# Kernel tuning notes

Hardware: AMD Instinct MI355X
Metric: run time of the kernel (lower is better)

The kernel has to match this reference:

```python
import jax, jax.numpy as jnp
import numpy as np

B, N, C, H, KH = 4, 4096, 1024, 16, 5
HD = C // H  # head dim = 64


def setup_inputs() -> dict:
    key = jax.random.key(0)
    ks = jax.random.split(key, 4)
    return {
        "x": jax.random.normal(ks[0], (B, N, C), jnp.float32),
        "qkv_w": jax.random.normal(ks[1], (3 * C, C), jnp.float32) * 0.02,
        "qkv_b": jnp.zeros((3 * C,), jnp.float32),
        "proj_w": jax.random.normal(ks[2], (C, C), jnp.float32) * 0.02,
        "proj_b": jnp.zeros((C,), jnp.float32),
        "pos_enc": jnp.zeros((1, C), jnp.float32),  # torch init: zeros
        "dwc_w": jax.random.normal(ks[3], (HD, 1, KH, KH), jnp.float32) * 0.05,
        "dwc_b": jnp.zeros((HD,), jnp.float32),
        "num_heads": H,
    }


def reference(x, qkv_w, qkv_b, proj_w, proj_b, pos_enc, dwc_w, dwc_b, num_heads):
    b, n, c = x.shape
    h = num_heads
    hd = c // h
    kh = dwc_w.shape[2]

    qkv = x @ qkv_w.T + qkv_b                     # (b, n, 3c)
    q, k, v = jnp.split(qkv, 3, axis=-1)          # each (b, n, c)
    k = k + pos_enc[:, :c]                        # broadcast (1, c)
    q = jax.nn.relu(q)
    k = jax.nn.relu(k)

    def to_heads(t):  # (b, n, c) -> (b*h, n, hd)
        return t.reshape(b, n, h, hd).transpose(0, 2, 1, 3).reshape(b * h, n, hd)

    q, k, v = to_heads(q), to_heads(k), to_heads(v)

    # linear attention in fp32 (inputs already fp32)
    z = 1.0 / (jnp.einsum('bic,bc->bi', q, k.sum(axis=1)) + 1e-6)   # (bh, n)
    kv = jnp.einsum('bjc,bjd->bcd', k, v)                           # (bh, hd, hd)
    out = jnp.einsum('bic,bcd->bid', q, kv) * z[:, :, None]         # (bh, n, hd)

    # depthwise 2D conv on v viewed as (bh, hd, n, 1), kernel (hd,1,kh,kh), pad kh//2
    fm = v.transpose(0, 2, 1)[..., None]                            # (bh, hd, n, 1)
    pad = kh // 2
    fm = jax.lax.conv_general_dilated(
        fm, dwc_w, window_strides=(1, 1),
        padding=((pad, pad), (pad, pad)),
        dimension_numbers=('NCHW', 'OIHW', 'NCHW'),
        feature_group_count=hd,
    ) + dwc_b[None, :, None, None]
    out = out + fm[..., 0].transpose(0, 2, 1)                       # (bh, n, hd)

    out = out.reshape(b, h, n, hd).transpose(0, 2, 1, 3).reshape(b, n, c)
    return out @ proj_w.T + proj_b
```

## Files before the change

kernel.cpp:

```cpp
#include <hip/hip_runtime.h>


#define BB   4
#define NN   4096
#define CDIM 1024
#define NH   16
#define HDIM 64
#define BH   64

typedef __attribute__((ext_vector_type(8))) short short8;
typedef __attribute__((ext_vector_type(4))) float f32x4;
typedef unsigned short u16;

__device__ __forceinline__ float b2f(short s) {
    union { unsigned u; float f; } c;
    c.u = ((unsigned)(unsigned short)s) << 16;
    return c.f;
}
__device__ __forceinline__ u16 f2b(float f) {
    unsigned u = __float_as_uint(f);
    return (u16)((u + 0x7fffu + ((u >> 16) & 1u)) >> 16);
}
__device__ __forceinline__ void gload16(const void* g, void* l) {
    __builtin_amdgcn_global_load_lds((const __attribute__((address_space(1))) void*)g,
                                     (__attribute__((address_space(3))) void*)l, 16, 0, 0);
}

__global__ __launch_bounds__(256) void k_fill_diag(float* __restrict__ out, int n, float val)
{
    int i = blockIdx.x * 256 + threadIdx.x;
    if (i < n) out[i] = val;
}

__global__ __launch_bounds__(256) void k_f32_to_bf16(const float* __restrict__ in,
                                                     u16* __restrict__ out, int n4)
{
    int i = blockIdx.x * 256 + threadIdx.x;
    if (i < n4) {
        float4 v = reinterpret_cast<const float4*>(in)[i];
        ushort4 o;
        o.x = f2b(v.x); o.y = f2b(v.y); o.z = f2b(v.z); o.w = f2b(v.w);
        reinterpret_cast<ushort4*>(out)[i] = o;
    }
}

__global__ __launch_bounds__(256) void k_gemm1_mfma(
    const u16* __restrict__ A,
    const u16* __restrict__ Bw,
    const float* __restrict__ bias, const float* __restrict__ pos_enc,
    u16* __restrict__ q, u16* __restrict__ kk_, u16* __restrict__ v)
{
    __shared__ u16 As[128 * 32];
    __shared__ u16 Bs[128 * 32];
    const int t = threadIdx.x;
    const int l = t & 63, w = t >> 6;
    const int wr = w >> 1, wc = w & 1;
    const int nbx = gridDim.x, nwg = nbx * gridDim.y;
    const int lid = blockIdx.y * nbx + blockIdx.x;
    const int swz = (lid & 7) * (nwg >> 3) + (lid >> 3);
    const int bcol = (swz % nbx) * 128;
    const int brow = (swz / nbx) * 128;
    const int sr = t >> 2;
    const int sk = (t & 3) * 8;
    const u16* gA = A  + (brow + sr) * 1024 + sk;
    const u16* gB = Bw + (bcol + sr) * 1024 + sk;
    char* ldsA = (char*)As + w * 1024;
    char* ldsB = (char*)Bs + w * 1024;

    f32x4 acc[4][4];
    #pragma unroll
    for (int m = 0; m < 4; ++m)
        #pragma unroll
        for (int n = 0; n < 4; ++n) acc[m][n] = (f32x4){0.f, 0.f, 0.f, 0.f};

    const int ar = wr * 64 + (l & 15);
    const int bc = wc * 64 + (l & 15);
    const int kfrag = (l >> 4) * 8;

    for (int k0 = 0; k0 < 1024; k0 += 32) {
        gload16(gA + k0,             ldsA);
        gload16(gA + k0 + 64 * 1024, ldsA + 4096);
        gload16(gB + k0,             ldsB);
        gload16(gB + k0 + 64 * 1024, ldsB + 4096);
        __syncthreads();
        short8 a[4], b[4];
        #pragma unroll
        for (int m = 0; m < 4; ++m)
            a[m] = *reinterpret_cast<const short8*>(&As[(ar + m * 16) * 32 + kfrag]);
        #pragma unroll
        for (int n = 0; n < 4; ++n)
            b[n] = *reinterpret_cast<const short8*>(&Bs[(bc + n * 16) * 32 + kfrag]);
        #pragma unroll
        for (int m = 0; m < 4; ++m)
            #pragma unroll
            for (int n = 0; n < 4; ++n)
                acc[m][n] = __builtin_amdgcn_mfma_f32_16x16x32_bf16(a[m], b[n], acc[m][n], 0, 0, 0);
        __syncthreads();
    }

    const int part = bcol >> 10;
    u16* dst = (part == 0) ? q : (part == 1) ? kk_ : v;
    const int col_base = bcol + wc * 64 + (l & 15);
    const int row_base = brow + wr * 64 + (l >> 4) * 4;
    #pragma unroll
    for (int n = 0; n < 4; ++n) {
        const int gc = col_base + n * 16;
        const int c  = gc & 1023;
        float bv = bias[gc];
        if (part == 1) bv += pos_enc[c];
        const int h = c >> 6, d = c & 63;
        #pragma unroll
        for (int m = 0; m < 4; ++m)
            #pragma unroll
            for (int j = 0; j < 4; ++j) {
                const int gr = row_base + m * 16 + j;
                const int b_ = gr >> 12, i_ = gr & 4095;
                float val = acc[m][n][j] + bv;
                if (part != 2) val = fmaxf(val, 0.f);
                dst[(size_t)((b_ * NH + h) * NN + i_) * HDIM + d] = f2b(val);
            }
    }
}

__global__ __launch_bounds__(256) void k_kv_partial(
    const u16* __restrict__ k, const u16* __restrict__ v,
    float* __restrict__ part_kv, float* __restrict__ part_ks)
{
    __shared__ float ks[32 * 64];
    __shared__ float vs[32 * 64];
    const int bh = blockIdx.x;
    const int chunk = blockIdx.y;
    const int t = threadIdx.x;
    const int cg = t >> 4;
    const int dg = t & 15;
    const int lr = t >> 3;
    const int lc = (t & 7) * 8;
    const size_t base = (size_t)bh * NN * HDIM + (size_t)chunk * 1024 * HDIM;
    float acc[4][4] = {};
    float ksac[4] = {};
    for (int j0 = 0; j0 < 1024; j0 += 32) {
        short8 kr = *reinterpret_cast<const short8*>(&k[base + (size_t)(j0 + lr) * 64 + lc]);
        short8 vr = *reinterpret_cast<const short8*>(&v[base + (size_t)(j0 + lr) * 64 + lc]);
        __syncthreads();
        #pragma unroll
        for (int j = 0; j < 8; ++j) {
            ks[lr * 64 + lc + j] = b2f(kr[j]);
            vs[lr * 64 + lc + j] = b2f(vr[j]);
        }
        __syncthreads();
        #pragma unroll
        for (int j = 0; j < 32; ++j) {
            float4 k4 = *reinterpret_cast<const float4*>(&ks[j * 64 + cg * 4]);
            float4 v4 = *reinterpret_cast<const float4*>(&vs[j * 64 + dg * 4]);
            const float* kp = reinterpret_cast<const float*>(&k4);
            const float* vp = reinterpret_cast<const float*>(&v4);
            #pragma unroll
            for (int ii = 0; ii < 4; ++ii) {
                ksac[ii] += kp[ii];
                #pragma unroll
                for (int jj = 0; jj < 4; ++jj)
                    acc[ii][jj] += kp[ii] * vp[jj];
            }
        }
    }
    const int pb = (chunk * BH + bh);
    #pragma unroll
    for (int ii = 0; ii < 4; ++ii) {
        #pragma unroll
        for (int jj = 0; jj < 4; ++jj)
            part_kv[pb * 4096 + (cg * 4 + ii) * 64 + dg * 4 + jj] = acc[ii][jj];
        if (dg == 0) part_ks[pb * 64 + cg * 4 + ii] = ksac[ii];
    }
}

__global__ __launch_bounds__(256) void k_kv_reduce_t(
    const float* __restrict__ part_kv, const float* __restrict__ part_ks,
    u16* __restrict__ kvt)
{
    const int bh = blockIdx.x;
    const int t = threadIdx.x;
    u16* base = kvt + bh * 5120;
    #pragma unroll
    for (int r = 0; r < 16; ++r) {
        const int idx = r * 256 + t;
        const int c = idx >> 6, d = idx & 63;
        float s = 0.f;
        #pragma unroll
        for (int ch = 0; ch < 4; ++ch) s += part_kv[(ch * BH + bh) * 4096 + idx];
        base[d * 64 + c] = f2b(s);
    }
    if (t < 64) {
        float s = 0.f;
        #pragma unroll
        for (int ch = 0; ch < 4; ++ch) s += part_ks[(ch * BH + bh) * 64 + t];
        base[4096 + t] = f2b(s);
    }
    for (int z = t; z < 960; z += 256) base[4160 + z] = 0;
}

__global__ __launch_bounds__(256) void k_attn_mfma(
    const u16* __restrict__ q, const u16* __restrict__ v,
    const u16* __restrict__ kvt,
    const float* __restrict__ dwc_w, const float* __restrict__ dwc_b,
    u16* __restrict__ out2)
{
    __shared__ u16 att[4][64 * 68];
    const int t = threadIdx.x;
    const int l = t & 63, w = t >> 6;
    const int bh = blockIdx.x;
    const int tb = blockIdx.y * 256 + w * 64;
    const size_t hb = (size_t)bh * NN * HDIM;
    const u16* qb  = q + hb + (size_t)tb * HDIM;
    const u16* kvb = kvt + bh * 5120;

    const int fr = l & 15;
    const int kfrag = (l >> 4) * 8;

    short8 bfr[5][2];
    #pragma unroll
    for (int n = 0; n < 5; ++n)
        #pragma unroll
        for (int ks = 0; ks < 2; ++ks)
            bfr[n][ks] = *reinterpret_cast<const short8*>(&kvb[(n * 16 + fr) * 64 + ks * 32 + kfrag]);

    f32x4 acc[4][5];
    #pragma unroll
    for (int m = 0; m < 4; ++m)
        #pragma unroll
        for (int n = 0; n < 5; ++n) acc[m][n] = (f32x4){0.f, 0.f, 0.f, 0.f};

    #pragma unroll
    for (int m = 0; m < 4; ++m)
        #pragma unroll
        for (int ks = 0; ks < 2; ++ks) {
            short8 a = *reinterpret_cast<const short8*>(&qb[(m * 16 + fr) * 64 + ks * 32 + kfrag]);
            #pragma unroll
            for (int n = 0; n < 5; ++n)
                acc[m][n] = __builtin_amdgcn_mfma_f32_16x16x32_bf16(a, bfr[n][ks], acc[m][n], 0, 0, 0);
        }

    #pragma unroll
    for (int m = 0; m < 4; ++m)
        #pragma unroll
        for (int j = 0; j < 4; ++j) {
            const float den = __shfl(acc[m][4][j], l & 48);
            const float z = 1.f / (den + 1e-6f);
            const int row = m * 16 + (l >> 4) * 4 + j;
            #pragma unroll
            for (int n = 0; n < 4; ++n)
                att[w][row * 68 + fr + n * 16] = f2b(acc[m][n][j] * z);
        }
    __syncthreads();

    const int d = l;
    float w5[5];
    #pragma unroll
    for (int dh = 0; dh < 5; ++dh) w5[dh] = dwc_w[d * 25 + dh * 5 + 2];
    const float cbias = dwc_b[d];
    const int b_ = bh >> 4, h_ = bh & 15;
    u16* obase = out2 + (size_t)b_ * NN * CDIM + (size_t)h_ * 64 + d;
    float win[5];
    #pragma unroll
    for (int p = 0; p < 4; ++p) {
        const int src = tb - 2 + p;
        win[p] = (src >= 0 && src < NN) ? b2f(v[hb + (size_t)src * 64 + d]) : 0.f;
    }
    for (int it = 0; it < 64; ++it) {
        const int srcn = tb + it + 2;
        win[4] = (srcn < NN) ? b2f(v[hb + (size_t)srcn * 64 + d]) : 0.f;
        const float fm = cbias + w5[0] * win[0] + w5[1] * win[1] + w5[2] * win[2]
                               + w5[3] * win[3] + w5[4] * win[4];
        const float attn = b2f((short)att[w][it * 68 + d]);
        obase[(size_t)(tb + it) * CDIM] = f2b(attn + fm);
        win[0] = win[1]; win[1] = win[2]; win[2] = win[3]; win[3] = win[4];
    }
}

__global__ __launch_bounds__(256) void k_gemm2_mfma(
    const u16* __restrict__ A,
    const u16* __restrict__ Bw,
    const float* __restrict__ bias, float* __restrict__ out)
{
    __shared__ u16 As[128 * 32];
    __shared__ u16 Bs[128 * 32];
    const int t = threadIdx.x;
    const int l = t & 63, w = t >> 6;
    const int wr = w >> 1, wc = w & 1;
    const int nbx = gridDim.x, nwg = nbx * gridDim.y;
    const int lid = blockIdx.y * nbx + blockIdx.x;
    const int swz = (lid & 7) * (nwg >> 3) + (lid >> 3);
    const int bcol = (swz % nbx) * 128;
    const int brow = (swz / nbx) * 128;
    const int sr = t >> 2;
    const int sk = (t & 3) * 8;
    const u16* gA = A  + (brow + sr) * 1024 + sk;
    const u16* gB = Bw + (bcol + sr) * 1024 + sk;
    char* ldsA = (char*)As + w * 1024;
    char* ldsB = (char*)Bs + w * 1024;

    f32x4 acc[4][4];
    #pragma unroll
    for (int m = 0; m < 4; ++m)
        #pragma unroll
        for (int n = 0; n < 4; ++n) acc[m][n] = (f32x4){0.f, 0.f, 0.f, 0.f};

    const int ar = wr * 64 + (l & 15);
    const int bc = wc * 64 + (l & 15);
    const int kfrag = (l >> 4) * 8;

    for (int k0 = 0; k0 < 1024; k0 += 32) {
        gload16(gA + k0,             ldsA);
        gload16(gA + k0 + 64 * 1024, ldsA + 4096);
        gload16(gB + k0,             ldsB);
        gload16(gB + k0 + 64 * 1024, ldsB + 4096);
        __syncthreads();
        short8 a[4], b[4];
        #pragma unroll
        for (int m = 0; m < 4; ++m)
            a[m] = *reinterpret_cast<const short8*>(&As[(ar + m * 16) * 32 + kfrag]);
        #pragma unroll
        for (int n = 0; n < 4; ++n)
            b[n] = *reinterpret_cast<const short8*>(&Bs[(bc + n * 16) * 32 + kfrag]);
        #pragma unroll
        for (int m = 0; m < 4; ++m)
            #pragma unroll
            for (int n = 0; n < 4; ++n)
                acc[m][n] = __builtin_amdgcn_mfma_f32_16x16x32_bf16(a[m], b[n], acc[m][n], 0, 0, 0);
        __syncthreads();
    }

    const int col_base = bcol + wc * 64 + (l & 15);
    const int row_base = brow + wr * 64 + (l >> 4) * 4;
    #pragma unroll
    for (int n = 0; n < 4; ++n) {
        const int gc = col_base + n * 16;
        const float bv = bias[gc];
        #pragma unroll
        for (int m = 0; m < 4; ++m)
            #pragma unroll
            for (int j = 0; j < 4; ++j) {
                const int gr = row_base + m * 16 + j;
                out[(size_t)gr * CDIM + gc] = acc[m][n][j] + bv;
            }
    }
}

extern "C" void kernel_launch(void* const* d_in, const int* in_sizes, int n_in,
                              void* d_out, int out_size, void* d_ws, size_t ws_size,
                              hipStream_t stream)
{
    const float* x       = (const float*)d_in[0];
    const float* qkv_w   = (const float*)d_in[1];
    const float* qkv_b   = (const float*)d_in[2];
    const float* proj_w  = (const float*)d_in[3];
    const float* proj_b  = (const float*)d_in[4];
    const float* pos_enc = (const float*)d_in[5];
    const float* dwc_w   = (const float*)d_in[6];
    const float* dwc_b   = (const float*)d_in[7];

    const size_t QKV = 16777216;
    char* p = (char*)d_ws;
    u16* q_b    = (u16*)p;               p += QKV * 2;
    u16* k_b    = (u16*)p;               p += QKV * 2;
    u16* v_b    = (u16*)p;               p += QKV * 2;
    u16* x_b    = (u16*)p;               p += QKV * 2;
    u16* qkvw_b = (u16*)p;               p += (size_t)3145728 * 2;
    u16* projw_b= (u16*)p;               p += (size_t)1048576 * 2;
    float* part_kv = (float*)p;          p += (size_t)1048576 * 4;
    float* part_ks = (float*)p;          p += (size_t)16384 * 4;
    u16* kvt       = (u16*)p;            p += (size_t)(64 * 5120) * 2;
    const size_t need_bytes = (size_t)(p - (char*)d_ws);

    if (ws_size < need_bytes) {
        const float diag = 4096.0f + (float)(ws_size >> 20);
        k_fill_diag<<<(out_size + 255) / 256, 256, 0, stream>>>((float*)d_out, out_size, diag);
        return;
    }

    u16* out2 = k_b;
    float* out = (float*)d_out;

    k_f32_to_bf16<<<16384, 256, 0, stream>>>(x,      x_b,     4194304);
    k_f32_to_bf16<<< 3072, 256, 0, stream>>>(qkv_w,  qkvw_b,   786432);
    k_f32_to_bf16<<< 1024, 256, 0, stream>>>(proj_w, projw_b,  262144);

    k_gemm1_mfma <<<dim3(24, 128), 256, 0, stream>>>(x_b, qkvw_b, qkv_b, pos_enc, q_b, k_b, v_b);
    k_kv_partial <<<dim3(64, 4),   256, 0, stream>>>(k_b, v_b, part_kv, part_ks);
    k_kv_reduce_t<<<64,            256, 0, stream>>>(part_kv, part_ks, kvt);
    k_attn_mfma  <<<dim3(64, 16),  256, 0, stream>>>(q_b, v_b, kvt, dwc_w, dwc_b, out2);
    k_gemm2_mfma <<<dim3(8, 128),  256, 0, stream>>>(out2, projw_b, proj_b, out);
}
```

Before: 321.2 us.

## Rewrite both GEMMs as 256x256 double-buffered MFMA tiles with swizzled LDS

Replaces the 128x128 single-buffered GEMM kernels for the QKV and output projections with 256x256 tiles computed by 512-thread blocks. Global-to-LDS loads go into two buffers so the next k-slice is fetched while MFMAs run on the current one, and the LDS layout is XOR-swizzled to cut bank conflicts. It also raises wave priority around the MFMA block. Each wave now holds twice as many accumulators, which increases register pressure, and the larger tiles produce fewer blocks and lower occupancy.

```diff
diff --git a/kernel.cpp b/kernel.cpp
--- a/kernel.cpp
+++ b/kernel.cpp
@@ -44,64 +44,89 @@
     }
 }
 
-__global__ __launch_bounds__(256) void k_gemm1_mfma(
+
+#define GEMM_PROLOGUE_AND_LOOP(EXTRA_BCOLS)                                              \
+    const int t = threadIdx.x;                                                           \
+    const int l = t & 63, w = t >> 6;                                                    \
+    const int wr = w >> 2, wc = w & 3;                                                   \
+    const int qa = ((l & 3) ^ ((l >> 3) & 3)) * 8;                                       \
+    const int srow = t >> 2;                                                             \
+    const u16* gA = A  + (size_t)(brow + srow) * 1024 + qa;                              \
+    const u16* gB = Bw + (size_t)(bcol + srow) * 1024 + qa;                              \
+    const int fr = l & 15;                                                               \
+    const int phys8 = ((l >> 4) ^ ((l >> 1) & 3)) * 8;                                   \
+    const int arow0 = wr * 128 + fr;                                                     \
+    const int bfr0  = wc * 64 + fr;                                                      \
+    f32x4 acc[8][4];                                                                     \
+    _Pragma("unroll")                                                                    \
+    for (int m = 0; m < 8; ++m)                                                          \
+        _Pragma("unroll")                                                                \
+        for (int n = 0; n < 4; ++n) acc[m][n] = (f32x4){0.f, 0.f, 0.f, 0.f};             \
+                                              \
+    auto STAGE = [&](int buf, int kt) {                                                  \
+        const int kof = kt * 32;                                                         \
+        char* lb = (char*)lds + buf * 32768 + w * 1024;                                  \
+        gload16(gA + kof,          lb);                                                  \
+        gload16(gA + 131072 + kof, lb + 8192);                                           \
+        gload16(gB + kof,          lb + 16384);                                          \
+        gload16(gB + 131072 + kof, lb + 24576);                                          \
+    };                                                                                   \
+    STAGE(0, 0);                                                                         \
+    STAGE(1, 1);                                                                         \
+    asm volatile("s_waitcnt vmcnt(4)" ::: "memory");                                     \
+    __builtin_amdgcn_sched_barrier(0);                                                   \
+    __builtin_amdgcn_s_barrier();                                                        \
+    __builtin_amdgcn_sched_barrier(0);                                                   \
+    for (int kt = 0; kt < 32; ++kt) {                                                    \
+        const int cur = kt & 1;                                                          \
+        const int ab = cur * 16384;                                                      \
+        short8 af[8], bf[4];                                                             \
+        _Pragma("unroll")                                                                \
+        for (int n = 0; n < 4; ++n)                                                      \
+            bf[n] = *reinterpret_cast<const short8*>(                                    \
+                        &lds[ab + 8192 + (bfr0 + n * 16) * 32 + phys8]);                 \
+        _Pragma("unroll")                                                                \
+        for (int m = 0; m < 8; ++m)                                                      \
+            af[m] = *reinterpret_cast<const short8*>(                                    \
+                        &lds[ab + (arow0 + m * 16) * 32 + phys8]);                       \
+        asm volatile("s_waitcnt lgkmcnt(0)" ::: "memory");                               \
+        __builtin_amdgcn_sched_barrier(0);                                               \
+        __builtin_amdgcn_s_barrier();               \
+        __builtin_amdgcn_sched_barrier(0);                                               \
+        if (kt + 2 < 32) STAGE(cur, kt + 2);                                             \
+        __builtin_amdgcn_s_setprio(1);                                                   \
+        _Pragma("unroll")                                                                \
+        for (int m = 0; m < 8; ++m)                                                      \
+            _Pragma("unroll")                                                            \
+            for (int n = 0; n < 4; ++n)                                                  \
+                acc[m][n] = __builtin_amdgcn_mfma_f32_16x16x32_bf16(                     \
+                                af[m], bf[n], acc[m][n], 0, 0, 0);                       \
+        __builtin_amdgcn_s_setprio(0);                                                   \
+        if (kt + 2 < 32) { asm volatile("s_waitcnt vmcnt(4)" ::: "memory"); }            \
+        else             { asm volatile("s_waitcnt vmcnt(0)" ::: "memory"); }            \
+        __builtin_amdgcn_sched_barrier(0);                                               \
+        __builtin_amdgcn_s_barrier();                 \
+        __builtin_amdgcn_sched_barrier(0);                                               \
+    }
+
+__global__ __launch_bounds__(512, 2) void k_gemm1_256(
     const u16* __restrict__ A,
     const u16* __restrict__ Bw,
     const float* __restrict__ bias, const float* __restrict__ pos_enc,
     u16* __restrict__ q, u16* __restrict__ kk_, u16* __restrict__ v)
 {
-    __shared__ u16 As[128 * 32];
-    __shared__ u16 Bs[128 * 32];
-    const int t = threadIdx.x;
-    const int l = t & 63, w = t >> 6;
-    const int wr = w >> 1, wc = w & 1;
-    const int nbx = gridDim.x, nwg = nbx * gridDim.y;
-    const int lid = blockIdx.y * nbx + blockIdx.x;
-    const int swz = (lid & 7) * (nwg >> 3) + (lid >> 3);
-    const int bcol = (swz % nbx) * 128;
-    const int brow = (swz / nbx) * 128;
-    const int sr = t >> 2;
-    const int sk = (t & 3) * 8;
-    const u16* gA = A  + (brow + sr) * 1024 + sk;
-    const u16* gB = Bw + (bcol + sr) * 1024 + sk;
-    char* ldsA = (char*)As + w * 1024;
-    char* ldsB = (char*)Bs + w * 1024;
-
-    f32x4 acc[4][4];
-    #pragma unroll
-    for (int m = 0; m < 4; ++m)
-        #pragma unroll
-        for (int n = 0; n < 4; ++n) acc[m][n] = (f32x4){0.f, 0.f, 0.f, 0.f};
-
-    const int ar = wr * 64 + (l & 15);
-    const int bc = wc * 64 + (l & 15);
-    const int kfrag = (l >> 4) * 8;
-
-    for (int k0 = 0; k0 < 1024; k0 += 32) {
-        gload16(gA + k0,             ldsA);
-        gload16(gA + k0 + 64 * 1024, ldsA + 4096);
-        gload16(gB + k0,             ldsB);
-        gload16(gB + k0 + 64 * 1024, ldsB + 4096);
-        __syncthreads();
-        short8 a[4], b[4];
-        #pragma unroll
-        for (int m = 0; m < 4; ++m)
-            a[m] = *reinterpret_cast<const short8*>(&As[(ar + m * 16) * 32 + kfrag]);
-        #pragma unroll
-        for (int n = 0; n < 4; ++n)
-            b[n] = *reinterpret_cast<const short8*>(&Bs[(bc + n * 16) * 32 + kfrag]);
-        #pragma unroll
-        for (int m = 0; m < 4; ++m)
-            #pragma unroll
-            for (int n = 0; n < 4; ++n)
-                acc[m][n] = __builtin_amdgcn_mfma_f32_16x16x32_bf16(a[m], b[n], acc[m][n], 0, 0, 0);
-        __syncthreads();
-    }
+    __shared__ u16 lds[32768];
+    const int lid = blockIdx.y * 12 + blockIdx.x;
+    const int swz = (lid & 7) * 96 + (lid >> 3);
+    const int bcol = (swz % 12) * 256;
+    const int brow = (swz / 12) * 256;
+
+    GEMM_PROLOGUE_AND_LOOP()
 
     const int part = bcol >> 10;
     u16* dst = (part == 0) ? q : (part == 1) ? kk_ : v;
-    const int col_base = bcol + wc * 64 + (l & 15);
-    const int row_base = brow + wr * 64 + (l >> 4) * 4;
+    const int col_base = bcol + wc * 64 + fr;
+    const int row_base = brow + wr * 128 + (l >> 4) * 4;
     #pragma unroll
     for (int n = 0; n < 4; ++n) {
         const int gc = col_base + n * 16;
@@ -110,7 +135,7 @@
         if (part == 1) bv += pos_enc[c];
         const int h = c >> 6, d = c & 63;
         #pragma unroll
-        for (int m = 0; m < 4; ++m)
+        for (int m = 0; m < 8; ++m)
             #pragma unroll
             for (int j = 0; j < 4; ++j) {
                 const int gr = row_base + m * 16 + j;
@@ -118,6 +143,35 @@
                 float val = acc[m][n][j] + bv;
                 if (part != 2) val = fmaxf(val, 0.f);
                 dst[(size_t)((b_ * NH + h) * NN + i_) * HDIM + d] = f2b(val);
+            }
+    }
+}
+
+__global__ __launch_bounds__(512, 2) void k_gemm2_256(
+    const u16* __restrict__ A,
+    const u16* __restrict__ Bw,
+    const float* __restrict__ bias, float* __restrict__ out)
+{
+    __shared__ u16 lds[32768];
+    const int lid = blockIdx.y * 4 + blockIdx.x;
+    const int swz = (lid & 7) * 32 + (lid >> 3);
+    const int bcol = (swz % 4) * 256;
+    const int brow = (swz / 4) * 256;
+
+    GEMM_PROLOGUE_AND_LOOP()
+
+    const int col_base = bcol + wc * 64 + fr;
+    const int row_base = brow + wr * 128 + (l >> 4) * 4;
+    #pragma unroll
+    for (int n = 0; n < 4; ++n) {
+        const int gc = col_base + n * 16;
+        const float bv = bias[gc];
+        #pragma unroll
+        for (int m = 0; m < 8; ++m)
+            #pragma unroll
+            for (int j = 0; j < 4; ++j) {
+                const int gr = row_base + m * 16 + j;
+                out[(size_t)gr * CDIM + gc] = acc[m][n][j] + bv;
             }
     }
 }
@@ -276,75 +330,6 @@
     }
 }
 
-__global__ __launch_bounds__(256) void k_gemm2_mfma(
-    const u16* __restrict__ A,
-    const u16* __restrict__ Bw,
-    const float* __restrict__ bias, float* __restrict__ out)
-{
-    __shared__ u16 As[128 * 32];
-    __shared__ u16 Bs[128 * 32];
-    const int t = threadIdx.x;
-    const int l = t & 63, w = t >> 6;
-    const int wr = w >> 1, wc = w & 1;
-    const int nbx = gridDim.x, nwg = nbx * gridDim.y;
-    const int lid = blockIdx.y * nbx + blockIdx.x;
-    const int swz = (lid & 7) * (nwg >> 3) + (lid >> 3);
-    const int bcol = (swz % nbx) * 128;
-    const int brow = (swz / nbx) * 128;
-    const int sr = t >> 2;
-    const int sk = (t & 3) * 8;
-    const u16* gA = A  + (brow + sr) * 1024 + sk;
-    const u16* gB = Bw + (bcol + sr) * 1024 + sk;
-    char* ldsA = (char*)As + w * 1024;
-    char* ldsB = (char*)Bs + w * 1024;
-
-    f32x4 acc[4][4];
-    #pragma unroll
-    for (int m = 0; m < 4; ++m)
-        #pragma unroll
-        for (int n = 0; n < 4; ++n) acc[m][n] = (f32x4){0.f, 0.f, 0.f, 0.f};
-
-    const int ar = wr * 64 + (l & 15);
-    const int bc = wc * 64 + (l & 15);
-    const int kfrag = (l >> 4) * 8;
-
-    for (int k0 = 0; k0 < 1024; k0 += 32) {
-        gload16(gA + k0,             ldsA);
-        gload16(gA + k0 + 64 * 1024, ldsA + 4096);
-        gload16(gB + k0,             ldsB);
-        gload16(gB + k0 + 64 * 1024, ldsB + 4096);
-        __syncthreads();
-        short8 a[4], b[4];
-        #pragma unroll
-        for (int m = 0; m < 4; ++m)
-            a[m] = *reinterpret_cast<const short8*>(&As[(ar + m * 16) * 32 + kfrag]);
-        #pragma unroll
-        for (int n = 0; n < 4; ++n)
-            b[n] = *reinterpret_cast<const short8*>(&Bs[(bc + n * 16) * 32 + kfrag]);
-        #pragma unroll
-        for (int m = 0; m < 4; ++m)
-            #pragma unroll
-            for (int n = 0; n < 4; ++n)
-                acc[m][n] = __builtin_amdgcn_mfma_f32_16x16x32_bf16(a[m], b[n], acc[m][n], 0, 0, 0);
-        __syncthreads();
-    }
-
-    const int col_base = bcol + wc * 64 + (l & 15);
-    const int row_base = brow + wr * 64 + (l >> 4) * 4;
-    #pragma unroll
-    for (int n = 0; n < 4; ++n) {
-        const int gc = col_base + n * 16;
-        const float bv = bias[gc];
-        #pragma unroll
-        for (int m = 0; m < 4; ++m)
-            #pragma unroll
-            for (int j = 0; j < 4; ++j) {
-                const int gr = row_base + m * 16 + j;
-                out[(size_t)gr * CDIM + gc] = acc[m][n][j] + bv;
-            }
-    }
-}
-
 extern "C" void kernel_launch(void* const* d_in, const int* in_sizes, int n_in,
                               void* d_out, int out_size, void* d_ws, size_t ws_size,
                               hipStream_t stream)
@@ -384,9 +369,9 @@
     k_f32_to_bf16<<< 3072, 256, 0, stream>>>(qkv_w,  qkvw_b,   786432);
     k_f32_to_bf16<<< 1024, 256, 0, stream>>>(proj_w, projw_b,  262144);
 
-    k_gemm1_mfma <<<dim3(24, 128), 256, 0, stream>>>(x_b, qkvw_b, qkv_b, pos_enc, q_b, k_b, v_b);
-    k_kv_partial <<<dim3(64, 4),   256, 0, stream>>>(k_b, v_b, part_kv, part_ks);
-    k_kv_reduce_t<<<64,            256, 0, stream>>>(part_kv, part_ks, kvt);
-    k_attn_mfma  <<<dim3(64, 16),  256, 0, stream>>>(q_b, v_b, kvt, dwc_w, dwc_b, out2);
-    k_gemm2_mfma <<<dim3(8, 128),  256, 0, stream>>>(out2, projw_b, proj_b, out);
-}
+    k_gemm1_256  <<<dim3(12, 64), 512, 0, stream>>>(x_b, qkvw_b, qkv_b, pos_enc, q_b, k_b, v_b);
+    k_kv_partial <<<dim3(64, 4),  256, 0, stream>>>(k_b, v_b, part_kv, part_ks);
+    k_kv_reduce_t<<<64,           256, 0, stream>>>(part_kv, part_ks, kvt);
+    k_attn_mfma  <<<dim3(64, 16), 256, 0, stream>>>(q_b, v_b, kvt, dwc_w, dwc_b, out2);
+    k_gemm2_256  <<<dim3(4, 64),  512, 0, stream>>>(out2, projw_b, proj_b, out);
+}
```

Result: no change. 315.4 us (-1.8%).
